# Kernel optimization log

Hardware: AMD Instinct MI355X
Metric: run time of the kernel (lower is better)

Reference implementation:

```python
import jax, jax.numpy as jnp
import numpy as np

FRAME_LENGTH = 64
ATTENUATE_GAIN = 0.01


def setup_inputs() -> dict:
    key = jax.random.key(0)
    k1, k2 = jax.random.split(key)
    B, F, FC = 32, 4000, 65
    H = jax.random.uniform(k1, (B, F, FC), dtype=jnp.float32)
    noise = jax.random.uniform(k2, (B, F, FRAME_LENGTH), dtype=jnp.float32)
    return {"H": H, "noise": noise}


def reference(H, noise):
    B, F, fc = H.shape
    M = 2 * fc - 1                      # linear-phase IR length (129)
    L = M + FRAME_LENGTH - 1            # FFT conv length (192)

    # periodic hann window, matching torch.hann_window default
    win = 0.5 * (1.0 - jnp.cos(2.0 * jnp.pi * jnp.arange(M, dtype=jnp.float32) / M))

    # zero-phase FR -> zero-phase IR -> linear-phase windowed IR
    ir = jnp.fft.irfft(H.astype(jnp.complex64), n=M, axis=-1)  # (B, F, M)
    ir = jnp.roll(ir, fc - 1, axis=-1) * win

    # FFT-domain filtering (rfft with n=L zero-pads, same as explicit pad)
    IR = jnp.fft.rfft(ir, n=L, axis=-1)                        # (B, F, L//2+1)
    N = jnp.fft.rfft(noise * 2.0 - 1.0, n=L, axis=-1)          # (B, F, L//2+1)
    X = N * IR

    # Faithful to the original: irfft with n = number of BINS (97), which
    # trims the spectrum to n//2+1 bins and outputs n time samples.
    nb = X.shape[-1]                                           # 97
    y = jnp.fft.irfft(X, n=nb, axis=-1) * ATTENUATE_GAIN       # (B, F, nb)

    # overlap-add (equivalent to conv_transpose1d with identity kernel, stride=frame_length)
    out_len = (F - 1) * FRAME_LENGTH + nb
    idx = jnp.arange(F)[:, None] * FRAME_LENGTH + jnp.arange(nb)[None, :]  # (F, nb)
    out = jnp.zeros((B, out_len), dtype=y.dtype).at[:, idx].add(y)
    return out
```

## Files before the change

kernel.cpp:

```cpp
#include <hip/hip_runtime.h>
#include <math.h>

#define FC     65
#define NB     97
#define FRAME  64
#define B_     32
#define F_     4000
#define OUT_LEN ((F_ - 1) * FRAME + NB)
#define CHUNK  63
#define NCHUNK 64

#define KP     128
#define D_OFF  0
#define W_OFF  (64 * KP)
#define E_OFF  (129 * KP)
#define NROWS  226
#define GUARD_IDX (NROWS * KP)
#define MAGIC  0x5F3C0FEE

__global__ void fn_init(float* __restrict__ ws, int useGuard) {
    if (useGuard && ((const int*)ws)[GUARD_IDX] == MAGIC) return;
    int tid = blockIdx.x * blockDim.x + threadIdx.x;
    if (tid >= NROWS * KP) return;
    int row = tid >> 7;
    int fo  = tid & 127;
    int s   = fo >> 4;
    int w   = fo & 15;
    int slot = w >> 1, im = w & 1;
    int cnt  = (s == 0) ? 7 : 6;
    float val = 0.0f;
    if (slot < cnt) {
        int k = (s == 0) ? slot : (6 * s + 1 + slot);
        if (row < 64) {
            int j = row;
            double x = -(double)(k * j) / 96.0;
            val = im ? (float)sinpi(x) : (float)cospi(x);
        } else if (row < 129) {
            int kap = row - 64;
            double sr_ = cospi(-(double)k / 96.0), si_ = sinpi(-(double)k / 96.0);
            double er = 1.0, ei = 0.0;
            double C2 = 2.0 * cospi(2.0 * (double)kap / 129.0);
            double c_prev = cospi(-130.0 * (double)kap / 129.0);
            double c_cur  = cospi(-128.0 * (double)kap / 129.0);
            double U2 = 2.0 * cospi(2.0 / 129.0);
            double u_prev = cospi(2.0 / 129.0);
            double u_cur  = 1.0;
            double accr = 0.0, acci = 0.0;
            for (int m = 0; m < 129; m++) {
                double win = 0.5 * (1.0 - u_cur);
                double a = win * (1.0 / 129.0);
                if (kap) a *= 2.0 * c_cur;
                accr += a * er; acci += a * ei;
                double un = U2 * u_cur - u_prev; u_prev = u_cur; u_cur = un;
                double cn = C2 * c_cur - c_prev; c_prev = c_cur; c_cur = cn;
                double e2r = er * sr_ - ei * si_;
                double e2i = er * si_ + ei * sr_;
                er = e2r; ei = e2i;
            }
            val = im ? (float)acci : (float)accr;
        } else {
            int t = row - 129;
            double g = 0.01 / 97.0;
            double x = 2.0 * (double)(k * t) / 97.0;
            val = im ? (float)(k == 0 ? 0.0 : -2.0 * g * sinpi(x))
                     : (float)(g * (k == 0 ? 1.0 : 2.0) * cospi(x));
        }
    }
    ws[tid] = val;
}

__global__ void fn_seal(float* __restrict__ ws) { ((int*)ws)[GUARD_IDX] = MAGIC; }

__device__ __forceinline__ float dppx1(float x) {
    return __int_as_float(__builtin_amdgcn_mov_dpp(__float_as_int(x), 0xB1, 0xF, 0xF, false));
}
__device__ __forceinline__ float dppx2(float x) {
    return __int_as_float(__builtin_amdgcn_mov_dpp(__float_as_int(x), 0x4E, 0xF, 0xF, false));
}
__device__ __forceinline__ float dpphm(float x) {
    return __int_as_float(__builtin_amdgcn_mov_dpp(__float_as_int(x), 0x141, 0xF, 0xF, false));
}

#define FR8(M) M(0) M(1) M(2) M(3) M(4) M(5) M(6) M(7)

#define DXS(f,s) float Xr##f##_##s = 0.f, Xi##f##_##s = 0.f;
#define DXF(f) DXS(f,0) DXS(f,1) DXS(f,2) DXS(f,3) DXS(f,4) DXS(f,5) DXS(f,6)

#define P1S(f,nf,re,im,s) Xr##f##_##s = fmaf(nf,re,Xr##f##_##s); Xi##f##_##s = fmaf(nf,im,Xi##f##_##s);
#define P1F(f,nf,A,B,C,D) P1S(f,nf,A.x,A.y,0) P1S(f,nf,A.z,A.w,1) P1S(f,nf,B.x,B.y,2) \
  P1S(f,nf,B.z,B.w,3) P1S(f,nf,C.x,C.y,4) P1S(f,nf,C.z,C.w,5) P1S(f,nf,D.x,D.y,6)
#define P1ROW(A,B,C,D,na,nb) P1F(0,na.x,A,B,C,D) P1F(1,na.y,A,B,C,D) P1F(2,na.z,A,B,C,D) \
  P1F(3,na.w,A,B,C,D) P1F(4,nb.x,A,B,C,D) P1F(5,nb.y,A,B,C,D) P1F(6,nb.z,A,B,C,D) P1F(7,nb.w,A,B,C,D)

#define P3S(f,hf,re,im,s) Rr##f##_##s = fmaf(hf,re,Rr##f##_##s); Ri##f##_##s = fmaf(hf,im,Ri##f##_##s);
#define P3FA(f,hf,A,B) P3S(f,hf,A.x,A.y,0) P3S(f,hf,A.z,A.w,1) P3S(f,hf,B.x,B.y,2) P3S(f,hf,B.z,B.w,3)
#define P3ROWA(A,B,ha,hb) P3FA(0,ha.x,A,B) P3FA(1,ha.y,A,B) P3FA(2,ha.z,A,B) P3FA(3,ha.w,A,B) \
  P3FA(4,hb.x,A,B) P3FA(5,hb.y,A,B) P3FA(6,hb.z,A,B) P3FA(7,hb.w,A,B)
#define P3FB(f,hf,C,D) P3S(f,hf,C.x,C.y,4) P3S(f,hf,C.z,C.w,5) P3S(f,hf,D.x,D.y,6)
#define P3ROWB(C,D,ha,hb) P3FB(0,ha.x,C,D) P3FB(1,ha.y,C,D) P3FB(2,ha.z,C,D) P3FB(3,ha.w,C,D) \
  P3FB(4,hb.x,C,D) P3FB(5,hb.y,C,D) P3FB(6,hb.z,C,D) P3FB(7,hb.w,C,D)

#define P4S(f,s) { float xr_ = Xr##f##_##s*Rr##f##_##s - Xi##f##_##s*Ri##f##_##s; \
  Xi##f##_##s = Xr##f##_##s*Ri##f##_##s + Xi##f##_##s*Rr##f##_##s; Xr##f##_##s = xr_; }
#define P4FA(f) P4S(f,0) P4S(f,1) P4S(f,2) P4S(f,3)
#define P4FB(f) P4S(f,4) P4S(f,5) P4S(f,6)

#define P5S(f,re,im,s) y##f = fmaf(Xr##f##_##s,re,y##f); y##f = fmaf(Xi##f##_##s,im,y##f);
#define P5F(f,A,B,C,D) P5S(f,A.x,A.y,0) P5S(f,A.z,A.w,1) P5S(f,B.x,B.y,2) P5S(f,B.z,B.w,3) \
  P5S(f,C.x,C.y,4) P5S(f,C.z,C.w,5) P5S(f,D.x,D.y,6)
#define P5ROW(A,B,C,D) P5F(0,A,B,C,D) P5F(1,A,B,C,D) P5F(2,A,B,C,D) P5F(3,A,B,C,D) \
  P5F(4,A,B,C,D) P5F(5,A,B,C,D) P5F(6,A,B,C,D) P5F(7,A,B,C,D)

#define P5REDUCE \
    float m0, m1, m2, m3, n0, n1, ym; \
    { float a_=(kg&4)?y4:y0, b_=(kg&4)?y0:y4; m0 = a_ + dpphm(b_); } \
    { float a_=(kg&4)?y5:y1, b_=(kg&4)?y1:y5; m1 = a_ + dpphm(b_); } \
    { float a_=(kg&4)?y6:y2, b_=(kg&4)?y2:y6; m2 = a_ + dpphm(b_); } \
    { float a_=(kg&4)?y7:y3, b_=(kg&4)?y3:y7; m3 = a_ + dpphm(b_); } \
    { float a_=(kg&2)?m2:m0, b_=(kg&2)?m0:m2; n0 = a_ + dppx2(b_); } \
    { float a_=(kg&2)?m3:m1, b_=(kg&2)?m1:m3; n1 = a_ + dppx2(b_); } \
    { float a_=(kg&1)?n1:n0, b_=(kg&1)?n0:n1; ym = a_ + dppx1(b_); }

#define OLA(t_) \
    if ((t_) < 64) { \
        if (L) buf[(L - 1) * 65 + (t_)] = ym; \
    } else { \
        int rr = (t_) - 64; \
        if (L < 63) buf[L * 65 + rr] += ym; \
        if (isLast) out[lastBase + (t_)] = ym; \
    }

__launch_bounds__(64, 2)
__global__ void fn_main_kernel(const float* __restrict__ H,
                               const float* __restrict__ noise,
                               const float* __restrict__ ws,
                               float* __restrict__ out) {
    __shared__ __align__(16) float buf[65 * 68];

    int bid = blockIdx.x;
    int b = bid >> 6;
    int c = bid & 63;
    int f0 = c * CHUNK;
    int nf = (CHUNK < F_ - f0) ? CHUNK : (F_ - f0);
    int L = threadIdx.x;
    int kg = L & 7;
    int fg8 = L & 56;
    int isLast = (f0 - 1 + L == F_ - 1);
    long lastBase = (long)b * OUT_LEN + (long)(F_ - 1) * FRAME;

    long nbase = ((long)b * F_ + (f0 - 1)) * FRAME + (long)L * FRAME;
    const long nmax = (long)B_ * F_ * FRAME - 4;
#pragma unroll 1
    for (int s4 = 0; s4 < 16; s4++) {
        long g = nbase + 4 * s4;
        g = g < 0 ? 0 : (g > nmax ? nmax : g);
        float4 v = *(const float4*)(noise + g);
        float4 w4;
        w4.x = fmaf(2.0f, v.x, -1.0f); w4.y = fmaf(2.0f, v.y, -1.0f);
        w4.z = fmaf(2.0f, v.z, -1.0f); w4.w = fmaf(2.0f, v.w, -1.0f);
        if (c == 0 && L == 0) { w4.x = w4.y = w4.z = w4.w = 0.0f; }
        int s0 = 4 * s4;
        buf[(s0 + 0) * 68 + L] = w4.x;
        buf[(s0 + 1) * 68 + L] = w4.y;
        buf[(s0 + 2) * 68 + L] = w4.z;
        buf[(s0 + 3) * 68 + L] = w4.w;
    }
    __syncthreads();

    FR8(DXF)

    {
        const float* dp = ws + D_OFF + kg * 16;
        float4 a0, a1, a2, a3, b0, b1, b2, b3;
        { const float4* q = (const float4*)dp; a0 = q[0]; a1 = q[1]; a2 = q[2]; a3 = q[3]; }
#pragma unroll 1
        for (int j = 0; j < 64; j += 2) {
            { const float4* q = (const float4*)(dp + (j + 1) * KP); b0 = q[0]; b1 = q[1]; b2 = q[2]; b3 = q[3]; }
            float4 na = *(const float4*)(buf + j * 68 + fg8);
            float4 nb = *(const float4*)(buf + j * 68 + fg8 + 4);
            P1ROW(a0, a1, a2, a3, na, nb)
            if (j + 2 < 64) { const float4* q = (const float4*)(dp + (j + 2) * KP); a0 = q[0]; a1 = q[1]; a2 = q[2]; a3 = q[3]; }
            na = *(const float4*)(buf + (j + 1) * 68 + fg8);
            nb = *(const float4*)(buf + (j + 1) * 68 + fg8 + 4);
            P1ROW(b0, b1, b2, b3, na, nb)
        }
    }
    __syncthreads();

    long hbase = ((long)b * F_ + (f0 - 1)) * FC + (long)L * FC;
    const long hmax = (long)B_ * F_ * FC - 1;
#pragma unroll 1
    for (int kap = 0; kap < 65; kap++) {
        long g = hbase + kap;
        g = g < 0 ? 0 : (g > hmax ? hmax : g);
        buf[kap * 68 + L] = H[g];
    }
    __syncthreads();

    {
#define DRFA(f) float Rr##f##_0=0.f,Ri##f##_0=0.f,Rr##f##_1=0.f,Ri##f##_1=0.f, \
                      Rr##f##_2=0.f,Ri##f##_2=0.f,Rr##f##_3=0.f,Ri##f##_3=0.f;
        FR8(DRFA)
#undef DRFA
        const float* wp = ws + W_OFF + kg * 16;
        float4 a0, a1, b0, b1;
        { const float4* q = (const float4*)wp; a0 = q[0]; a1 = q[1]; }
#pragma unroll 1
        for (int r = 0; r < 65; r += 2) {
            if (r + 1 < 65) { const float4* q = (const float4*)(wp + (r + 1) * KP); b0 = q[0]; b1 = q[1]; }
            float4 ha = *(const float4*)(buf + r * 68 + fg8);
            float4 hb = *(const float4*)(buf + r * 68 + fg8 + 4);
            P3ROWA(a0, a1, ha, hb)
            if (r + 2 < 65) { const float4* q = (const float4*)(wp + (r + 2) * KP); a0 = q[0]; a1 = q[1]; }
            if (r + 1 < 65) {
                ha = *(const float4*)(buf + (r + 1) * 68 + fg8);
                hb = *(const float4*)(buf + (r + 1) * 68 + fg8 + 4);
                P3ROWA(b0, b1, ha, hb)
            }
        }
        FR8(P4FA)
    }
    {
#define DRFB(f) float Rr##f##_4=0.f,Ri##f##_4=0.f,Rr##f##_5=0.f,Ri##f##_5=0.f, \
                      Rr##f##_6=0.f,Ri##f##_6=0.f;
        FR8(DRFB)
#undef DRFB
        const float* wp = ws + W_OFF + kg * 16;
        float4 c0, c1, d0, d1;
        { const float4* q = (const float4*)wp; c0 = q[2]; c1 = q[3]; }
#pragma unroll 1
        for (int r = 0; r < 65; r += 2) {
            if (r + 1 < 65) { const float4* q = (const float4*)(wp + (r + 1) * KP); d0 = q[2]; d1 = q[3]; }
            float4 ha = *(const float4*)(buf + r * 68 + fg8);
            float4 hb = *(const float4*)(buf + r * 68 + fg8 + 4);
            P3ROWB(c0, c1, ha, hb)
            if (r + 2 < 65) { const float4* q = (const float4*)(wp + (r + 2) * KP); c0 = q[2]; c1 = q[3]; }
            if (r + 1 < 65) {
                ha = *(const float4*)(buf + (r + 1) * 68 + fg8);
                hb = *(const float4*)(buf + (r + 1) * 68 + fg8 + 4);
                P3ROWB(d0, d1, ha, hb)
            }
        }
        FR8(P4FB)
    }
    __syncthreads();

    {
        const float* ep = ws + E_OFF + kg * 16;
        float4 a0, a1, a2, a3, b0, b1, b2, b3;
        { const float4* q = (const float4*)ep; a0 = q[0]; a1 = q[1]; a2 = q[2]; a3 = q[3]; }
#pragma unroll 1
        for (int t = 0; t < 97; t += 2) {
            if (t + 1 < 97) { const float4* q = (const float4*)(ep + (t + 1) * KP); b0 = q[0]; b1 = q[1]; b2 = q[2]; b3 = q[3]; }
            {
                float y0=0.f,y1=0.f,y2=0.f,y3=0.f,y4=0.f,y5=0.f,y6=0.f,y7=0.f;
                P5ROW(a0, a1, a2, a3)
                P5REDUCE
                OLA(t)
            }
            if (t + 2 < 97) { const float4* q = (const float4*)(ep + (t + 2) * KP); a0 = q[0]; a1 = q[1]; a2 = q[2]; a3 = q[3]; }
            if (t + 1 < 97) {
                float y0=0.f,y1=0.f,y2=0.f,y3=0.f,y4=0.f,y5=0.f,y6=0.f,y7=0.f;
                P5ROW(b0, b1, b2, b3)
                P5REDUCE
                OLA(t + 1)
            }
        }
    }
    __syncthreads();

    long obase2 = (long)b * OUT_LEN + (long)f0 * FRAME;
#pragma unroll 1
    for (int i = 0; i < nf; i++) {
        out[obase2 + (long)i * 64 + L] = buf[i * 65 + L];
    }
}

extern "C" void kernel_launch(void* const* d_in, const int* in_sizes, int n_in,
                              void* d_out, int out_size, void* d_ws, size_t ws_size,
                              hipStream_t stream) {
    const float* H     = (const float*)d_in[0];
    const float* noise = (const float*)d_in[1];
    float* out = (float*)d_out;
    float* ws  = (float*)d_ws;

    int useGuard = (ws_size >= (size_t)(NROWS * KP + 1) * sizeof(float)) ? 1 : 0;
    fn_init<<<(NROWS * KP + 255) / 256, 256, 0, stream>>>(ws, useGuard);
    fn_main_kernel<<<B_ * NCHUNK, 64, 0, stream>>>(H, noise, ws, out);
    if (useGuard) fn_seal<<<1, 1, 0, stream>>>(ws);
}
```

Baseline: 246.2 us.

## Split each chunk block across two wavefronts with four frames per thread

Doubles the block to 128 threads so each thread handles four frames instead of eight. Noise loading, H loading and output writeback are divided between the two wavefronts, and the DPP reduction loses one level. The OLA stage is split into head and tail loops with a barrier between them, so the tail's accumulate into buf does not race with the other wavefront's writes. This cuts per-thread register pressure and raises occupancy (launch bounds 128,4). The cost is duplicated coefficient loads per wave and an extra sync.

Result: slower. 325.0 us (+32.0%).

```diff
diff --git a/kernel.cpp b/kernel.cpp
--- a/kernel.cpp
+++ b/kernel.cpp
@@ -81,7 +81,7 @@
     return __int_as_float(__builtin_amdgcn_mov_dpp(__float_as_int(x), 0x141, 0xF, 0xF, false));
 }
 
-#define FR8(M) M(0) M(1) M(2) M(3) M(4) M(5) M(6) M(7)
+#define FR4(M) M(0) M(1) M(2) M(3)
 
 #define DXS(f,s) float Xr##f##_##s = 0.f, Xi##f##_##s = 0.f;
 #define DXF(f) DXS(f,0) DXS(f,1) DXS(f,2) DXS(f,3) DXS(f,4) DXS(f,5) DXS(f,6)
@@ -89,16 +89,13 @@
 #define P1S(f,nf,re,im,s) Xr##f##_##s = fmaf(nf,re,Xr##f##_##s); Xi##f##_##s = fmaf(nf,im,Xi##f##_##s);
 #define P1F(f,nf,A,B,C,D) P1S(f,nf,A.x,A.y,0) P1S(f,nf,A.z,A.w,1) P1S(f,nf,B.x,B.y,2) \
   P1S(f,nf,B.z,B.w,3) P1S(f,nf,C.x,C.y,4) P1S(f,nf,C.z,C.w,5) P1S(f,nf,D.x,D.y,6)
-#define P1ROW(A,B,C,D,na,nb) P1F(0,na.x,A,B,C,D) P1F(1,na.y,A,B,C,D) P1F(2,na.z,A,B,C,D) \
-  P1F(3,na.w,A,B,C,D) P1F(4,nb.x,A,B,C,D) P1F(5,nb.y,A,B,C,D) P1F(6,nb.z,A,B,C,D) P1F(7,nb.w,A,B,C,D)
+#define P1ROW(A,B,C,D,na) P1F(0,na.x,A,B,C,D) P1F(1,na.y,A,B,C,D) P1F(2,na.z,A,B,C,D) P1F(3,na.w,A,B,C,D)
 
 #define P3S(f,hf,re,im,s) Rr##f##_##s = fmaf(hf,re,Rr##f##_##s); Ri##f##_##s = fmaf(hf,im,Ri##f##_##s);
 #define P3FA(f,hf,A,B) P3S(f,hf,A.x,A.y,0) P3S(f,hf,A.z,A.w,1) P3S(f,hf,B.x,B.y,2) P3S(f,hf,B.z,B.w,3)
-#define P3ROWA(A,B,ha,hb) P3FA(0,ha.x,A,B) P3FA(1,ha.y,A,B) P3FA(2,ha.z,A,B) P3FA(3,ha.w,A,B) \
-  P3FA(4,hb.x,A,B) P3FA(5,hb.y,A,B) P3FA(6,hb.z,A,B) P3FA(7,hb.w,A,B)
+#define P3ROWA(A,B,ha) P3FA(0,ha.x,A,B) P3FA(1,ha.y,A,B) P3FA(2,ha.z,A,B) P3FA(3,ha.w,A,B)
 #define P3FB(f,hf,C,D) P3S(f,hf,C.x,C.y,4) P3S(f,hf,C.z,C.w,5) P3S(f,hf,D.x,D.y,6)
-#define P3ROWB(C,D,ha,hb) P3FB(0,ha.x,C,D) P3FB(1,ha.y,C,D) P3FB(2,ha.z,C,D) P3FB(3,ha.w,C,D) \
-  P3FB(4,hb.x,C,D) P3FB(5,hb.y,C,D) P3FB(6,hb.z,C,D) P3FB(7,hb.w,C,D)
+#define P3ROWB(C,D,ha) P3FB(0,ha.x,C,D) P3FB(1,ha.y,C,D) P3FB(2,ha.z,C,D) P3FB(3,ha.w,C,D)
 
 #define P4S(f,s) { float xr_ = Xr##f##_##s*Rr##f##_##s - Xi##f##_##s*Ri##f##_##s; \
   Xi##f##_##s = Xr##f##_##s*Ri##f##_##s + Xi##f##_##s*Rr##f##_##s; Xr##f##_##s = xr_; }
@@ -108,29 +105,24 @@
 #define P5S(f,re,im,s) y##f = fmaf(Xr##f##_##s,re,y##f); y##f = fmaf(Xi##f##_##s,im,y##f);
 #define P5F(f,A,B,C,D) P5S(f,A.x,A.y,0) P5S(f,A.z,A.w,1) P5S(f,B.x,B.y,2) P5S(f,B.z,B.w,3) \
   P5S(f,C.x,C.y,4) P5S(f,C.z,C.w,5) P5S(f,D.x,D.y,6)
-#define P5ROW(A,B,C,D) P5F(0,A,B,C,D) P5F(1,A,B,C,D) P5F(2,A,B,C,D) P5F(3,A,B,C,D) \
-  P5F(4,A,B,C,D) P5F(5,A,B,C,D) P5F(6,A,B,C,D) P5F(7,A,B,C,D)
+#define P5ROW(A,B,C,D) P5F(0,A,B,C,D) P5F(1,A,B,C,D) P5F(2,A,B,C,D) P5F(3,A,B,C,D)
 
 #define P5REDUCE \
-    float m0, m1, m2, m3, n0, n1, ym; \
-    { float a_=(kg&4)?y4:y0, b_=(kg&4)?y0:y4; m0 = a_ + dpphm(b_); } \
-    { float a_=(kg&4)?y5:y1, b_=(kg&4)?y1:y5; m1 = a_ + dpphm(b_); } \
-    { float a_=(kg&4)?y6:y2, b_=(kg&4)?y2:y6; m2 = a_ + dpphm(b_); } \
-    { float a_=(kg&4)?y7:y3, b_=(kg&4)?y3:y7; m3 = a_ + dpphm(b_); } \
+    float m0 = y0 + dpphm(y0); \
+    float m1 = y1 + dpphm(y1); \
+    float m2 = y2 + dpphm(y2); \
+    float m3 = y3 + dpphm(y3); \
+    float n0, n1, ym; \
     { float a_=(kg&2)?m2:m0, b_=(kg&2)?m0:m2; n0 = a_ + dppx2(b_); } \
     { float a_=(kg&2)?m3:m1, b_=(kg&2)?m1:m3; n1 = a_ + dppx2(b_); } \
     { float a_=(kg&1)?n1:n0, b_=(kg&1)?n0:n1; ym = a_ + dppx1(b_); }
 
-#define OLA(t_) \
-    if ((t_) < 64) { \
-        if (L) buf[(L - 1) * 65 + (t_)] = ym; \
-    } else { \
-        int rr = (t_) - 64; \
-        if (L < 63) buf[L * 65 + rr] += ym; \
-        if (isLast) out[lastBase + (t_)] = ym; \
-    }
-
-__launch_bounds__(64, 2)
+#define OLAH(t_) if (kg < 4 && so) buf[(so - 1) * 65 + (t_)] = ym;
+#define OLAT(t_) if (kg < 4) { int rr = (t_) - 64; \
+    if (so < 63) buf[so * 65 + rr] += ym; \
+    if (isLast) out[lastBase + (t_)] = ym; }
+
+__launch_bounds__(128, 4)
 __global__ void fn_main_kernel(const float* __restrict__ H,
                                const float* __restrict__ noise,
                                const float* __restrict__ ws,
@@ -142,32 +134,38 @@
     int c = bid & 63;
     int f0 = c * CHUNK;
     int nf = (CHUNK < F_ - f0) ? CHUNK : (F_ - f0);
-    int L = threadIdx.x;
+    int T  = threadIdx.x;
+    int wv = T >> 6;
+    int L  = T & 63;
     int kg = L & 7;
-    int fg8 = L & 56;
-    int isLast = (f0 - 1 + L == F_ - 1);
+    int fs = 32 * wv + 4 * (L >> 3);
+    int so = fs + kg;
+    int isLast = (kg < 4) && (f0 - 1 + so == F_ - 1);
     long lastBase = (long)b * OUT_LEN + (long)(F_ - 1) * FRAME;
 
-    long nbase = ((long)b * F_ + (f0 - 1)) * FRAME + (long)L * FRAME;
-    const long nmax = (long)B_ * F_ * FRAME - 4;
-#pragma unroll 1
-    for (int s4 = 0; s4 < 16; s4++) {
-        long g = nbase + 4 * s4;
-        g = g < 0 ? 0 : (g > nmax ? nmax : g);
-        float4 v = *(const float4*)(noise + g);
-        float4 w4;
-        w4.x = fmaf(2.0f, v.x, -1.0f); w4.y = fmaf(2.0f, v.y, -1.0f);
-        w4.z = fmaf(2.0f, v.z, -1.0f); w4.w = fmaf(2.0f, v.w, -1.0f);
-        if (c == 0 && L == 0) { w4.x = w4.y = w4.z = w4.w = 0.0f; }
-        int s0 = 4 * s4;
-        buf[(s0 + 0) * 68 + L] = w4.x;
-        buf[(s0 + 1) * 68 + L] = w4.y;
-        buf[(s0 + 2) * 68 + L] = w4.z;
-        buf[(s0 + 3) * 68 + L] = w4.w;
-    }
-    __syncthreads();
-
-    FR8(DXF)
+    {
+        int slot = T >> 1, half = T & 1;
+        long nbase = ((long)b * F_ + (f0 - 1)) * FRAME + (long)slot * FRAME + half * 32;
+        const long nmax = (long)B_ * F_ * FRAME - 4;
+#pragma unroll 1
+        for (int s4 = 0; s4 < 8; s4++) {
+            long g = nbase + 4 * s4;
+            g = g < 0 ? 0 : (g > nmax ? nmax : g);
+            float4 v = *(const float4*)(noise + g);
+            float4 w4;
+            w4.x = fmaf(2.0f, v.x, -1.0f); w4.y = fmaf(2.0f, v.y, -1.0f);
+            w4.z = fmaf(2.0f, v.z, -1.0f); w4.w = fmaf(2.0f, v.w, -1.0f);
+            if (c == 0 && slot == 0) { w4.x = w4.y = w4.z = w4.w = 0.0f; }
+            int s0 = half * 32 + 4 * s4;
+            buf[(s0 + 0) * 68 + slot] = w4.x;
+            buf[(s0 + 1) * 68 + slot] = w4.y;
+            buf[(s0 + 2) * 68 + slot] = w4.z;
+            buf[(s0 + 3) * 68 + slot] = w4.w;
+        }
+    }
+    __syncthreads();
+
+    FR4(DXF)
 
     {
         const float* dp = ws + D_OFF + kg * 16;
@@ -176,31 +174,32 @@
 #pragma unroll 1
         for (int j = 0; j < 64; j += 2) {
             { const float4* q = (const float4*)(dp + (j + 1) * KP); b0 = q[0]; b1 = q[1]; b2 = q[2]; b3 = q[3]; }
-            float4 na = *(const float4*)(buf + j * 68 + fg8);
-            float4 nb = *(const float4*)(buf + j * 68 + fg8 + 4);
-            P1ROW(a0, a1, a2, a3, na, nb)
+            float4 na = *(const float4*)(buf + j * 68 + fs);
+            P1ROW(a0, a1, a2, a3, na)
             if (j + 2 < 64) { const float4* q = (const float4*)(dp + (j + 2) * KP); a0 = q[0]; a1 = q[1]; a2 = q[2]; a3 = q[3]; }
-            na = *(const float4*)(buf + (j + 1) * 68 + fg8);
-            nb = *(const float4*)(buf + (j + 1) * 68 + fg8 + 4);
-            P1ROW(b0, b1, b2, b3, na, nb)
-        }
-    }
-    __syncthreads();
-
-    long hbase = ((long)b * F_ + (f0 - 1)) * FC + (long)L * FC;
-    const long hmax = (long)B_ * F_ * FC - 1;
-#pragma unroll 1
-    for (int kap = 0; kap < 65; kap++) {
-        long g = hbase + kap;
-        g = g < 0 ? 0 : (g > hmax ? hmax : g);
-        buf[kap * 68 + L] = H[g];
+            na = *(const float4*)(buf + (j + 1) * 68 + fs);
+            P1ROW(b0, b1, b2, b3, na)
+        }
+    }
+    __syncthreads();
+
+    {
+        long hbase = ((long)b * F_ + (f0 - 1)) * FC + (long)L * FC;
+        const long hmax = (long)B_ * F_ * FC - 1;
+        int k0 = wv ? 33 : 0, k1 = wv ? 65 : 33;
+#pragma unroll 1
+        for (int kap = k0; kap < k1; kap++) {
+            long g = hbase + kap;
+            g = g < 0 ? 0 : (g > hmax ? hmax : g);
+            buf[kap * 68 + L] = H[g];
+        }
     }
     __syncthreads();
 
     {
 #define DRFA(f) float Rr##f##_0=0.f,Ri##f##_0=0.f,Rr##f##_1=0.f,Ri##f##_1=0.f, \
                       Rr##f##_2=0.f,Ri##f##_2=0.f,Rr##f##_3=0.f,Ri##f##_3=0.f;
-        FR8(DRFA)
+        FR4(DRFA)
 #undef DRFA
         const float* wp = ws + W_OFF + kg * 16;
         float4 a0, a1, b0, b1;
@@ -208,22 +207,20 @@
 #pragma unroll 1
         for (int r = 0; r < 65; r += 2) {
             if (r + 1 < 65) { const float4* q = (const float4*)(wp + (r + 1) * KP); b0 = q[0]; b1 = q[1]; }
-            float4 ha = *(const float4*)(buf + r * 68 + fg8);
-            float4 hb = *(const float4*)(buf + r * 68 + fg8 + 4);
-            P3ROWA(a0, a1, ha, hb)
+            float4 ha = *(const float4*)(buf + r * 68 + fs);
+            P3ROWA(a0, a1, ha)
             if (r + 2 < 65) { const float4* q = (const float4*)(wp + (r + 2) * KP); a0 = q[0]; a1 = q[1]; }
             if (r + 1 < 65) {
-                ha = *(const float4*)(buf + (r + 1) * 68 + fg8);
-                hb = *(const float4*)(buf + (r + 1) * 68 + fg8 + 4);
-                P3ROWA(b0, b1, ha, hb)
-            }
-        }
-        FR8(P4FA)
+                ha = *(const float4*)(buf + (r + 1) * 68 + fs);
+                P3ROWA(b0, b1, ha)
+            }
+        }
+        FR4(P4FA)
     }
     {
 #define DRFB(f) float Rr##f##_4=0.f,Ri##f##_4=0.f,Rr##f##_5=0.f,Ri##f##_5=0.f, \
                       Rr##f##_6=0.f,Ri##f##_6=0.f;
-        FR8(DRFB)
+        FR4(DRFB)
 #undef DRFB
         const float* wp = ws + W_OFF + kg * 16;
         float4 c0, c1, d0, d1;
@@ -231,17 +228,15 @@
 #pragma unroll 1
         for (int r = 0; r < 65; r += 2) {
             if (r + 1 < 65) { const float4* q = (const float4*)(wp + (r + 1) * KP); d0 = q[2]; d1 = q[3]; }
-            float4 ha = *(const float4*)(buf + r * 68 + fg8);
-            float4 hb = *(const float4*)(buf + r * 68 + fg8 + 4);
-            P3ROWB(c0, c1, ha, hb)
+            float4 ha = *(const float4*)(buf + r * 68 + fs);
+            P3ROWB(c0, c1, ha)
             if (r + 2 < 65) { const float4* q = (const float4*)(wp + (r + 2) * KP); c0 = q[2]; c1 = q[3]; }
             if (r + 1 < 65) {
-                ha = *(const float4*)(buf + (r + 1) * 68 + fg8);
-                hb = *(const float4*)(buf + (r + 1) * 68 + fg8 + 4);
-                P3ROWB(d0, d1, ha, hb)
-            }
-        }
-        FR8(P4FB)
+                ha = *(const float4*)(buf + (r + 1) * 68 + fs);
+                P3ROWB(d0, d1, ha)
+            }
+        }
+        FR4(P4FB)
     }
     __syncthreads();
 
@@ -250,20 +245,44 @@
         float4 a0, a1, a2, a3, b0, b1, b2, b3;
         { const float4* q = (const float4*)ep; a0 = q[0]; a1 = q[1]; a2 = q[2]; a3 = q[3]; }
 #pragma unroll 1
-        for (int t = 0; t < 97; t += 2) {
+        for (int t = 0; t < 64; t += 2) {
+            { const float4* q = (const float4*)(ep + (t + 1) * KP); b0 = q[0]; b1 = q[1]; b2 = q[2]; b3 = q[3]; }
+            {
+                float y0=0.f,y1=0.f,y2=0.f,y3=0.f;
+                P5ROW(a0, a1, a2, a3)
+                P5REDUCE
+                OLAH(t)
+            }
+            if (t + 2 < 64) { const float4* q = (const float4*)(ep + (t + 2) * KP); a0 = q[0]; a1 = q[1]; a2 = q[2]; a3 = q[3]; }
+            {
+                float y0=0.f,y1=0.f,y2=0.f,y3=0.f;
+                P5ROW(b0, b1, b2, b3)
+                P5REDUCE
+                OLAH(t + 1)
+            }
+        }
+    }
+    __syncthreads();
+
+    {
+        const float* ep = ws + E_OFF + kg * 16;
+        float4 a0, a1, a2, a3, b0, b1, b2, b3;
+        { const float4* q = (const float4*)(ep + 64 * KP); a0 = q[0]; a1 = q[1]; a2 = q[2]; a3 = q[3]; }
+#pragma unroll 1
+        for (int t = 64; t < 97; t += 2) {
             if (t + 1 < 97) { const float4* q = (const float4*)(ep + (t + 1) * KP); b0 = q[0]; b1 = q[1]; b2 = q[2]; b3 = q[3]; }
             {
-                float y0=0.f,y1=0.f,y2=0.f,y3=0.f,y4=0.f,y5=0.f,y6=0.f,y7=0.f;
+                float y0=0.f,y1=0.f,y2=0.f,y3=0.f;
                 P5ROW(a0, a1, a2, a3)
                 P5REDUCE
-                OLA(t)
+                OLAT(t)
             }
             if (t + 2 < 97) { const float4* q = (const float4*)(ep + (t + 2) * KP); a0 = q[0]; a1 = q[1]; a2 = q[2]; a3 = q[3]; }
             if (t + 1 < 97) {
-                float y0=0.f,y1=0.f,y2=0.f,y3=0.f,y4=0.f,y5=0.f,y6=0.f,y7=0.f;
+                float y0=0.f,y1=0.f,y2=0.f,y3=0.f;
                 P5ROW(b0, b1, b2, b3)
                 P5REDUCE
-                OLA(t + 1)
+                OLAT(t + 1)
             }
         }
     }
@@ -271,7 +290,7 @@
 
     long obase2 = (long)b * OUT_LEN + (long)f0 * FRAME;
 #pragma unroll 1
-    for (int i = 0; i < nf; i++) {
+    for (int i = wv; i < nf; i += 2) {
         out[obase2 + (long)i * 64 + L] = buf[i * 65 + L];
     }
 }
@@ -286,6 +305,6 @@
 
     int useGuard = (ws_size >= (size_t)(NROWS * KP + 1) * sizeof(float)) ? 1 : 0;
     fn_init<<<(NROWS * KP + 255) / 256, 256, 0, stream>>>(ws, useGuard);
-    fn_main_kernel<<<B_ * NCHUNK, 64, 0, stream>>>(H, noise, ws, out);
+    fn_main_kernel<<<B_ * NCHUNK, 128, 0, stream>>>(H, noise, ws, out);
     if (useGuard) fn_seal<<<1, 1, 0, stream>>>(ws);
 }
```
